# Performance work log

Measured on AMD Instinct MI355X. Metric: run time of the kernel, lower is better.

The kernel has to match this reference:

```python
import jax, jax.numpy as jnp
import numpy as np

BATCH, OBS_DIM = 131072, 1024
H1, H2, H3 = 512, 512, 256

def _init_linear(key, in_f, out_f):
    kw, kb = jax.random.split(key)
    bound = 1.0 / np.sqrt(in_f)
    W = jax.random.uniform(kw, (out_f, in_f), jnp.float32, -bound, bound)
    b = jax.random.uniform(kb, (out_f,), jnp.float32, -bound, bound)
    return W, b

def setup_inputs() -> dict:
    key = jax.random.key(0)
    k_obs, k1, k2, k3 = jax.random.split(key, 4)
    obs = jax.random.normal(k_obs, (BATCH, OBS_DIM), jnp.float32)
    W1, b1 = _init_linear(k1, OBS_DIM, H1)
    W2, b2 = _init_linear(k2, H1, H2)
    W3, b3 = _init_linear(k3, H2, H3)
    return {"obs": obs, "W1": W1, "b1": b1, "W2": W2, "b2": b2, "W3": W3, "b3": b3}

def reference(obs, W1, b1, W2, b2, W3, b3):
    # Linear(F->512) GELU Linear(512->512) GELU Linear(512->256) GELU
    gelu = lambda x: jax.nn.gelu(x, approximate=False)  # matches F.gelu default (erf)
    x = gelu(obs @ W1.T + b1)
    x = gelu(x @ W2.T + b2)
    x = gelu(x @ W3.T + b3)
    return x
```

## Files before the change

### kernel.cpp

```cpp
#include <hip/hip_runtime.h>
#include <hip/hip_bf16.h>
#include <math.h>
#include <cstdint>


typedef __bf16 bf16_t;
typedef __attribute__((ext_vector_type(8))) __bf16 bf16x8;
typedef __attribute__((ext_vector_type(4))) float f32x4;
typedef __attribute__((ext_vector_type(4))) unsigned short u16x4;

#define BK 64
#define TILE_ELEMS (256 * 64)

__device__ inline unsigned short f2bf_rne(float f) {
    unsigned int u = __builtin_bit_cast(unsigned int, f);
    u += 0x7fffu + ((u >> 16) & 1u);
    return (unsigned short)(u >> 16);
}

__device__ inline float gelu_erf(float x) {
    return 0.5f * x * (1.0f + erff(x * 0.7071067811865475f));
}

__device__ inline void gload_lds16(const void* g, void* l) {
    auto gp = reinterpret_cast<const __attribute__((address_space(1))) unsigned int*>(
        reinterpret_cast<uintptr_t>(g));
    auto lp = reinterpret_cast<__attribute__((address_space(3))) unsigned int*>(
        reinterpret_cast<uintptr_t>(l));
    __builtin_amdgcn_global_load_lds(gp, lp, 16, 0, 0);
}

#define LOADA(QM)                                                               \
    _Pragma("unroll") for (int i = 0; i < 4; ++i)                               \
    _Pragma("unroll") for (int s = 0; s < 2; ++s) {                             \
        const int r_ = wm + (QM) * 64 + i * 16 + lrow;                          \
        a_fr[i][s] = *(const bf16x8*)(cA + r_ * BK + (((s * 4 + quad) ^ swz) << 3)); \
    }

#define LOADB(DST, QN)                                                          \
    _Pragma("unroll") for (int j = 0; j < 2; ++j)                               \
    _Pragma("unroll") for (int s = 0; s < 2; ++s) {                             \
        const int r_ = wn + (QN) * 32 + j * 16 + lrow;                          \
        DST[j][s] = *(const bf16x8*)(cB + r_ * BK + (((s * 4 + quad) ^ swz) << 3)); \
    }

#define MMA16(QM, QN, BFR)                                                      \
    _Pragma("unroll") for (int i = 0; i < 4; ++i)                               \
    _Pragma("unroll") for (int j = 0; j < 2; ++j)                               \
    _Pragma("unroll") for (int s = 0; s < 2; ++s)                               \
        acc[(QM) * 4 + i][(QN) * 2 + j] = __builtin_amdgcn_mfma_f32_16x16x32_bf16( \
            a_fr[i][s], BFR[j][s], acc[(QM) * 4 + i][(QN) * 2 + j], 0, 0, 0);

template <bool OUT_BF16>
__global__ __launch_bounds__(512, 2)
void gemm_bias_gelu(const bf16_t* __restrict__ A,
                    const bf16_t* __restrict__ B,
                    const float* __restrict__ bias,
                    void* __restrict__ Cv,
                    int M, int N, int K)
{
    __shared__ __align__(16) bf16_t lA[2 * TILE_ELEMS];
    __shared__ __align__(16) bf16_t lB[2 * TILE_ELEMS];

    const int tid  = threadIdx.x;
    const int wave = tid >> 6;
    const int lane = tid & 63;
    const int lrow = lane & 15;
    const int quad = lane >> 4;
    const int swz  = lrow & 7;

    const int gx  = gridDim.x;
    const int nwg = gx * gridDim.y;
    int bid = blockIdx.y * gx + blockIdx.x;
    if ((nwg & 7) == 0) {
        const int cpx = nwg >> 3;
        bid = (bid & 7) * cpx + (bid >> 3);
    }
    const int col0 = (bid % gx) * 256;
    const int row0 = (bid / gx) * 256;

    const int wm = (wave >> 2) * 128;
    const int wn = (wave & 3) * 64;

    const int srow = lane >> 3;
    const int gchk = (lane & 7) ^ srow;

    const int NT = K >> 6;
    const bf16_t* A0p = A + (size_t)row0 * K;
    const bf16_t* B0p = B + (size_t)col0 * K;

    auto stage_half = [&](int tile, int half) {
        if (tile >= NT) return;
        const int k0   = tile << 6;
        const bool isA = half < 2;
        const int rb   = (half & 1) * 128 + wave * 16;
        const bf16_t* g = (isA ? A0p : B0p) + (size_t)(rb + srow) * K + k0 + gchk * 8;
        bf16_t* l = (isA ? lA : lB) + (tile & 1) * TILE_ELEMS + rb * BK;
        #pragma unroll
        for (int c = 0; c < 2; ++c) {
            gload_lds16(g, l);
            g += (size_t)8 * K;
            l += 8 * BK;
        }
    };

    f32x4  acc[8][4] = {};
    bf16x8 a_fr[4][2];
    bf16x8 b_fr0[2][2], b_fr1[2][2];

    stage_half(0, 2); stage_half(0, 3); stage_half(0, 0); stage_half(0, 1);
    stage_half(1, 2); stage_half(1, 3);
    asm volatile("s_waitcnt vmcnt(4)" ::: "memory");
    __builtin_amdgcn_s_barrier();

    for (int t = 0; t < NT; ++t) {
        const bf16_t* cA = lA + (t & 1) * TILE_ELEMS;
        const bf16_t* cB = lB + (t & 1) * TILE_ELEMS;

        stage_half(t + 1, 0);
        LOADA(0)
        LOADB(b_fr0, 0)
        __builtin_amdgcn_s_barrier();
        asm volatile("s_waitcnt lgkmcnt(0)" ::: "memory");
        __builtin_amdgcn_s_setprio(1);
        MMA16(0, 0, b_fr0)
        __builtin_amdgcn_s_setprio(0);
        __builtin_amdgcn_s_barrier();

        stage_half(t + 1, 1);
        LOADB(b_fr1, 1)
        __builtin_amdgcn_s_barrier();
        asm volatile("s_waitcnt lgkmcnt(0)" ::: "memory");
        __builtin_amdgcn_s_setprio(1);
        MMA16(0, 1, b_fr1)
        __builtin_amdgcn_s_setprio(0);
        __builtin_amdgcn_s_barrier();

        stage_half(t + 2, 2);
        LOADA(1)
        __builtin_amdgcn_s_barrier();
        asm volatile("s_waitcnt lgkmcnt(0)" ::: "memory");
        __builtin_amdgcn_s_setprio(1);
        MMA16(1, 0, b_fr0)
        __builtin_amdgcn_s_setprio(0);
        __builtin_amdgcn_s_barrier();

        stage_half(t + 2, 3);
        __builtin_amdgcn_s_setprio(1);
        MMA16(1, 1, b_fr1)
        __builtin_amdgcn_s_setprio(0);
        if (t + 2 < NT) {
            asm volatile("s_waitcnt vmcnt(4)" ::: "memory");
        } else {
            asm volatile("s_waitcnt vmcnt(0)" ::: "memory");
        }
        __builtin_amdgcn_s_barrier();
    }

    float bv[4];
    #pragma unroll
    for (int nj = 0; nj < 4; ++nj) bv[nj] = bias[col0 + wn + nj * 16 + lrow];

    #pragma unroll
    for (int mi = 0; mi < 8; ++mi) {
        #pragma unroll
        for (int r = 0; r < 4; ++r) {
            const size_t row = (size_t)(row0 + wm + mi * 16 + quad * 4 + r);
            #pragma unroll
            for (int nj = 0; nj < 4; ++nj) {
                const int col = col0 + wn + nj * 16 + lrow;
                float v = acc[mi][nj][r] + bv[nj];
                v = gelu_erf(v);
                if constexpr (OUT_BF16)
                    ((unsigned short*)Cv)[row * N + col] = f2bf_rne(v);
                else
                    ((float*)Cv)[row * N + col] = v;
            }
        }
    }
}

__global__ void cvt_f32_to_bf16(const float* __restrict__ s,
                                unsigned short* __restrict__ d, int n4)
{
    const int i = blockIdx.x * 256 + threadIdx.x;
    if (i < n4) {
        const float4 v = ((const float4*)s)[i];
        u16x4 h;
        h.x = f2bf_rne(v.x); h.y = f2bf_rne(v.y);
        h.z = f2bf_rne(v.z); h.w = f2bf_rne(v.w);
        ((u16x4*)d)[i] = h;
    }
}

extern "C" void kernel_launch(void* const* d_in, const int* in_sizes, int n_in,
                              void* d_out, int out_size, void* d_ws, size_t ws_size,
                              hipStream_t stream)
{
    const int BATCH = 131072, OBS = 1024, H1 = 512, H2 = 512, H3 = 256;

    const float* obs = (const float*)d_in[0];
    const float* W1  = (const float*)d_in[1];
    const float* b1  = (const float*)d_in[2];
    const float* W2  = (const float*)d_in[3];
    const float* b2  = (const float*)d_in[4];
    const float* W3  = (const float*)d_in[5];
    const float* b3  = (const float*)d_in[6];
    float* out = (float*)d_out;

    char* ws = (char*)d_ws;
    bf16_t* x1   = (bf16_t*)ws;
    bf16_t* x2   = (bf16_t*)(ws + (size_t)BATCH * H1 * 2);
    bf16_t* obsb = (bf16_t*)(ws + (size_t)BATCH * (H1 + H2) * 2);
    bf16_t* w1b  = obsb + (size_t)BATCH * OBS;
    bf16_t* w2b  = w1b + (size_t)H1 * OBS;
    bf16_t* w3b  = w2b + (size_t)H2 * H1;

    cvt_f32_to_bf16<<<dim3((H1 * OBS / 4 + 255) / 256), 256, 0, stream>>>(W1, (unsigned short*)w1b, H1 * OBS / 4);
    cvt_f32_to_bf16<<<dim3((H2 * H1 / 4 + 255) / 256), 256, 0, stream>>>(W2, (unsigned short*)w2b, H2 * H1 / 4);
    cvt_f32_to_bf16<<<dim3((H3 * H2 / 4 + 255) / 256), 256, 0, stream>>>(W3, (unsigned short*)w3b, H3 * H2 / 4);
    cvt_f32_to_bf16<<<dim3(BATCH * OBS / 4 / 256), 256, 0, stream>>>(obs, (unsigned short*)obsb, BATCH * OBS / 4);

    gemm_bias_gelu<true><<<dim3(H1 / 256, BATCH / 256), 512, 0, stream>>>(
        obsb, w1b, b1, x1, BATCH, H1, OBS);
    gemm_bias_gelu<true><<<dim3(H2 / 256, BATCH / 256), 512, 0, stream>>>(
        x1, w2b, b2, x2, BATCH, H2, H1);
    gemm_bias_gelu<false><<<dim3(H3 / 256, BATCH / 256), 512, 0, stream>>>(
        x2, w3b, b3, out, BATCH, H3, H2);
}
```

Baseline: 1.104 ms.

## Fuse fp32-to-bf16 conversion of observations into first GEMM's A-tile staging

Removes the separate conversion kernel for the 512MB fp32 observation matrix. The first GEMM now loads fp32 A tiles into registers, converts them to bf16 and writes them into swizzled LDS, interleaved with the MFMA phases. This avoids writing and re-reading a 256MB bf16 copy. In exchange the first GEMM reads fp32 (twice the bytes) through registers rather than direct-to-LDS loads. That adds register pressure (8 float4 per thread) and VALU conversion work inside the main loop. Tail tiles now clamp their loads instead of skipping them, so the vmcnt waits stay uniform.

```diff
diff --git a/kernel.cpp b/kernel.cpp
--- a/kernel.cpp
+++ b/kernel.cpp
@@ -51,9 +51,9 @@
         acc[(QM) * 4 + i][(QN) * 2 + j] = __builtin_amdgcn_mfma_f32_16x16x32_bf16( \
             a_fr[i][s], BFR[j][s], acc[(QM) * 4 + i][(QN) * 2 + j], 0, 0, 0);
 
-template <bool OUT_BF16>
+template <bool A_IS_FP32, bool OUT_BF16>
 __global__ __launch_bounds__(512, 2)
-void gemm_bias_gelu(const bf16_t* __restrict__ A,
+void gemm_bias_gelu(const void* __restrict__ Av,
                     const bf16_t* __restrict__ B,
                     const float* __restrict__ bias,
                     void* __restrict__ Cv,
@@ -85,22 +85,55 @@
     const int srow = lane >> 3;
     const int gchk = (lane & 7) ^ srow;
 
-    const int NT = K >> 6;
-    const bf16_t* A0p = A + (size_t)row0 * K;
+    const int NT    = K >> 6;
+    const int lastT = NT - 1;
+    const bf16_t* A0p = (const bf16_t*)Av + (size_t)row0 * K;
+    const float*  Afp = (const float*)Av + (size_t)row0 * K;
     const bf16_t* B0p = B + (size_t)col0 * K;
 
-    auto stage_half = [&](int tile, int half) {
-        if (tile >= NT) return;
-        const int k0   = tile << 6;
-        const bool isA = half < 2;
-        const int rb   = (half & 1) * 128 + wave * 16;
-        const bf16_t* g = (isA ? A0p : B0p) + (size_t)(rb + srow) * K + k0 + gchk * 8;
-        bf16_t* l = (isA ? lA : lB) + (tile & 1) * TILE_ELEMS + rb * BK;
+    auto stageB_half = [&](int tile, int half) {
+        const int st = tile < lastT ? tile : lastT;
+        const int k0 = st << 6;
+        const int rb = half * 128 + wave * 16;
+        const bf16_t* g = B0p + (size_t)(rb + srow) * K + k0 + gchk * 8;
+        bf16_t* l = lB + (tile & 1) * TILE_ELEMS + rb * BK;
+        gload_lds16(g, l);
+        gload_lds16(g + (size_t)8 * K, l + 8 * BK);
+    };
+    auto stageA_half_bf16 = [&](int tile, int half) {
+        const int st = tile < lastT ? tile : lastT;
+        const int k0 = st << 6;
+        const int rb = half * 128 + wave * 16;
+        const bf16_t* g = A0p + (size_t)(rb + srow) * K + k0 + gchk * 8;
+        bf16_t* l = lA + (tile & 1) * TILE_ELEMS + rb * BK;
+        gload_lds16(g, l);
+        gload_lds16(g + (size_t)8 * K, l + 8 * BK);
+    };
+
+    float4 av[8];
+    auto loadA_f32 = [&](int tile) {
+        const int st = tile < lastT ? tile : lastT;
+        const int k0 = st << 6;
         #pragma unroll
-        for (int c = 0; c < 2; ++c) {
-            gload_lds16(g, l);
-            g += (size_t)8 * K;
-            l += 8 * BK;
+        for (int c = 0; c < 8; ++c) {
+            const int e = c * 2048 + tid * 4;
+            const int r = e >> 6;
+            const int k = e & 63;
+            av[c] = *(const float4*)(Afp + (size_t)r * K + k0 + k);
+        }
+    };
+    auto writeA_f32_half = [&](int tile, int half) {
+        bf16_t* dst = lA + (tile & 1) * TILE_ELEMS;
+        #pragma unroll
+        for (int c = half * 4; c < half * 4 + 4; ++c) {
+            const int e = c * 2048 + tid * 4;
+            const int r = e >> 6;
+            const int k = e & 63;
+            u16x4 h;
+            h.x = f2bf_rne(av[c].x); h.y = f2bf_rne(av[c].y);
+            h.z = f2bf_rne(av[c].z); h.w = f2bf_rne(av[c].w);
+            const int off = r * BK + (((k >> 3) ^ (r & 7)) << 3) + (k & 7);
+            *(u16x4*)(dst + off) = h;
         }
     };
 
@@ -108,16 +141,26 @@
     bf16x8 a_fr[4][2];
     bf16x8 b_fr0[2][2], b_fr1[2][2];
 
-    stage_half(0, 2); stage_half(0, 3); stage_half(0, 0); stage_half(0, 1);
-    stage_half(1, 2); stage_half(1, 3);
+    stageB_half(0, 0); stageB_half(0, 1);
+    if constexpr (A_IS_FP32) {
+        loadA_f32(0);
+    } else {
+        stageA_half_bf16(0, 0); stageA_half_bf16(0, 1);
+    }
+    stageB_half(1, 0); stageB_half(1, 1);
     asm volatile("s_waitcnt vmcnt(4)" ::: "memory");
+    if constexpr (A_IS_FP32) {
+        writeA_f32_half(0, 0); writeA_f32_half(0, 1);
+        asm volatile("s_waitcnt lgkmcnt(0)" ::: "memory");
+    }
     __builtin_amdgcn_s_barrier();
 
     for (int t = 0; t < NT; ++t) {
         const bf16_t* cA = lA + (t & 1) * TILE_ELEMS;
         const bf16_t* cB = lB + (t & 1) * TILE_ELEMS;
 
-        stage_half(t + 1, 0);
+        if constexpr (A_IS_FP32) loadA_f32(t + 1);
+        else                     stageA_half_bf16(t + 1, 0);
         LOADA(0)
         LOADB(b_fr0, 0)
         __builtin_amdgcn_s_barrier();
@@ -127,7 +170,7 @@
         __builtin_amdgcn_s_setprio(0);
         __builtin_amdgcn_s_barrier();
 
-        stage_half(t + 1, 1);
+        if constexpr (!A_IS_FP32) stageA_half_bf16(t + 1, 1);
         LOADB(b_fr1, 1)
         __builtin_amdgcn_s_barrier();
         asm volatile("s_waitcnt lgkmcnt(0)" ::: "memory");
@@ -136,8 +179,12 @@
         __builtin_amdgcn_s_setprio(0);
         __builtin_amdgcn_s_barrier();
 
-        stage_half(t + 2, 2);
+        stageB_half(t + 2, 0);
         LOADA(1)
+        if constexpr (A_IS_FP32) {
+            asm volatile("s_waitcnt vmcnt(6)" ::: "memory");
+            writeA_f32_half(t + 1, 0);
+        }
         __builtin_amdgcn_s_barrier();
         asm volatile("s_waitcnt lgkmcnt(0)" ::: "memory");
         __builtin_amdgcn_s_setprio(1);
@@ -145,17 +192,18 @@
         __builtin_amdgcn_s_setprio(0);
         __builtin_amdgcn_s_barrier();
 
-        stage_half(t + 2, 3);
+        stageB_half(t + 2, 1);
         __builtin_amdgcn_s_setprio(1);
         MMA16(1, 1, b_fr1)
         __builtin_amdgcn_s_setprio(0);
-        if (t + 2 < NT) {
-            asm volatile("s_waitcnt vmcnt(4)" ::: "memory");
-        } else {
-            asm volatile("s_waitcnt vmcnt(0)" ::: "memory");
-        }
-        __builtin_amdgcn_s_barrier();
-    }
+        asm volatile("s_waitcnt vmcnt(4)" ::: "memory");
+        if constexpr (A_IS_FP32) {
+            writeA_f32_half(t + 1, 1);
+            asm volatile("s_waitcnt lgkmcnt(0)" ::: "memory");
+        }
+        __builtin_amdgcn_s_barrier();
+    }
+    asm volatile("s_waitcnt vmcnt(0)" ::: "memory");
 
     float bv[4];
     #pragma unroll
@@ -209,22 +257,20 @@
     float* out = (float*)d_out;
 
     char* ws = (char*)d_ws;
-    bf16_t* x1   = (bf16_t*)ws;
-    bf16_t* x2   = (bf16_t*)(ws + (size_t)BATCH * H1 * 2);
-    bf16_t* obsb = (bf16_t*)(ws + (size_t)BATCH * (H1 + H2) * 2);
-    bf16_t* w1b  = obsb + (size_t)BATCH * OBS;
-    bf16_t* w2b  = w1b + (size_t)H1 * OBS;
-    bf16_t* w3b  = w2b + (size_t)H2 * H1;
+    bf16_t* x1  = (bf16_t*)ws;
+    bf16_t* x2  = (bf16_t*)(ws + (size_t)BATCH * H1 * 2);
+    bf16_t* w1b = (bf16_t*)(ws + (size_t)BATCH * (H1 + H2) * 2);
+    bf16_t* w2b = w1b + (size_t)H1 * OBS;
+    bf16_t* w3b = w2b + (size_t)H2 * H1;
 
     cvt_f32_to_bf16<<<dim3((H1 * OBS / 4 + 255) / 256), 256, 0, stream>>>(W1, (unsigned short*)w1b, H1 * OBS / 4);
     cvt_f32_to_bf16<<<dim3((H2 * H1 / 4 + 255) / 256), 256, 0, stream>>>(W2, (unsigned short*)w2b, H2 * H1 / 4);
     cvt_f32_to_bf16<<<dim3((H3 * H2 / 4 + 255) / 256), 256, 0, stream>>>(W3, (unsigned short*)w3b, H3 * H2 / 4);
-    cvt_f32_to_bf16<<<dim3(BATCH * OBS / 4 / 256), 256, 0, stream>>>(obs, (unsigned short*)obsb, BATCH * OBS / 4);
-
-    gemm_bias_gelu<true><<<dim3(H1 / 256, BATCH / 256), 512, 0, stream>>>(
-        obsb, w1b, b1, x1, BATCH, H1, OBS);
-    gemm_bias_gelu<true><<<dim3(H2 / 256, BATCH / 256), 512, 0, stream>>>(
+
+    gemm_bias_gelu<true, true><<<dim3(H1 / 256, BATCH / 256), 512, 0, stream>>>(
+        obs, w1b, b1, x1, BATCH, H1, OBS);
+    gemm_bias_gelu<false, true><<<dim3(H2 / 256, BATCH / 256), 512, 0, stream>>>(
         x1, w2b, b2, x2, BATCH, H2, H1);
-    gemm_bias_gelu<false><<<dim3(H3 / 256, BATCH / 256), 512, 0, stream>>>(
+    gemm_bias_gelu<false, false><<<dim3(H3 / 256, BATCH / 256), 512, 0, stream>>>(
         x2, w3b, b3, out, BATCH, H3, H2);
 }
```

Measured after the change: 1.285 ms. 16.4% more time.
